# Performance work log

Hardware: AMD Instinct MI355X
Metric: run time of the kernel (lower is better)

Reference implementation:

```python
import jax, jax.numpy as jnp
import numpy as np
import math

D_MODEL = 1024
N_HEADS = 16
D_HEAD = D_MODEL // N_HEADS


def setup_inputs() -> dict:
    key = jax.random.key(0)
    ks = jax.random.split(key, 9)
    B, S = 4, 2048
    scale = 1.0 / math.sqrt(D_MODEL)
    x = jax.random.normal(ks[0], (B, S, D_MODEL), dtype=jnp.float32)
    # nn.Linear weights stored as [out, in]; we keep [in, out] for x @ W
    w_q = jax.random.uniform(ks[1], (D_MODEL, D_MODEL), jnp.float32, -scale, scale)
    b_q = jax.random.uniform(ks[2], (D_MODEL,), jnp.float32, -scale, scale)
    w_k = jax.random.uniform(ks[3], (D_MODEL, D_MODEL), jnp.float32, -scale, scale)
    b_k = jax.random.uniform(ks[4], (D_MODEL,), jnp.float32, -scale, scale)
    w_v = jax.random.uniform(ks[5], (D_MODEL, D_MODEL), jnp.float32, -scale, scale)
    b_v = jax.random.uniform(ks[6], (D_MODEL,), jnp.float32, -scale, scale)
    w_o = jax.random.uniform(ks[7], (D_MODEL, D_MODEL), jnp.float32, -scale, scale)
    b_o = jax.random.uniform(ks[8], (D_MODEL,), jnp.float32, -scale, scale)
    return {"x": x, "w_q": w_q, "b_q": b_q, "w_k": w_k, "b_k": b_k,
            "w_v": w_v, "b_v": b_v, "w_o": w_o, "b_o": b_o}


def reference(x, w_q, b_q, w_k, b_k, w_v, b_v, w_o, b_o):
    B, S, _ = x.shape
    def split_heads(t):  # [B,S,D] -> [B,H,S,Dh]
        return t.reshape(B, S, N_HEADS, D_HEAD).transpose(0, 2, 1, 3)
    q = split_heads(x @ w_q + b_q)
    k = split_heads(x @ w_k + b_k)
    v = split_heads(x @ w_v + b_v)
    scores = jnp.einsum('bhqd,bhkd->bhqk', q, k) / math.sqrt(D_HEAD)
    attn = jax.nn.softmax(scores, axis=-1)  # dropout p=0 -> identity
    ctx = jnp.einsum('bhqk,bhkd->bhqd', attn, v)
    ctx = ctx.transpose(0, 2, 1, 3).reshape(B, S, D_MODEL)
    return ctx @ w_o + b_o
```

## Files before the change

kernel.cpp:

```cpp
#include <hip/hip_runtime.h>
#include <hip/hip_bf16.h>

#define DM   1024
#define SEQ  2048
#define NH   16
#define DH   64
#define BH   64
#define MTOT 8192

typedef __attribute__((ext_vector_type(8))) short  short8;
typedef __attribute__((ext_vector_type(4))) short  short4v;
typedef __attribute__((ext_vector_type(4))) float  f32x4;
typedef __attribute__((ext_vector_type(4))) float  fvec4;
typedef unsigned short ushort_t;

#define AS1 __attribute__((address_space(1)))
#define AS3 __attribute__((address_space(3)))

static __device__ __forceinline__ unsigned short f2bf(float f){
  __bf16 h = (__bf16)f;
  return __builtin_bit_cast(unsigned short, h);
}

static __device__ __forceinline__ float fexp2(float x){
  float r;
  asm("v_exp_f32 %0, %1\n\ts_nop 0" : "=v"(r) : "v"(x));
  return r;
}

static __device__ __forceinline__ void gld16(const void* g, void* l){
  __builtin_amdgcn_global_load_lds((const AS1 int*)g, (AS3 int*)l, 16, 0, 0);
}

__global__ void k_cast_x(const float* __restrict__ x, ushort_t* __restrict__ xb){
  const size_t i = (size_t)blockIdx.x*256 + threadIdx.x;
  const fvec4* xv = (const fvec4*)x;
  fvec4 a = xv[2*i], b = xv[2*i+1];
  short8 r;
  #pragma unroll
  for (int j=0;j<4;++j) r[j]   = (short)f2bf(a[j]);
  #pragma unroll
  for (int j=0;j<4;++j) r[4+j] = (short)f2bf(b[j]);
  ((short8*)xb)[i] = r;
}

__global__ void k_cast_wt(const float* __restrict__ wq, const float* __restrict__ wk,
                          const float* __restrict__ wv, const float* __restrict__ wo,
                          ushort_t* __restrict__ wt){
  const int z = blockIdx.y;
  const float* W = (z==0)?wq:(z==1)?wk:(z==2)?wv:wo;
  ushort_t* Wt = wt + (size_t)z*DM*DM;
  const int k0 = (blockIdx.x & 15)*64, n0 = (blockIdx.x >> 4)*64;
  __shared__ float tile[64][65];
  const int t = threadIdx.x;
  #pragma unroll
  for (int it=0; it<4; ++it){
    int c = it*256 + t;
    int rr = c>>4, cc = c&15;
    fvec4 v = *(const fvec4*)(W + (size_t)(k0+rr)*DM + n0 + cc*4);
    #pragma unroll
    for (int j=0;j<4;++j) tile[cc*4+j][rr] = v[j];
  }
  __syncthreads();
  #pragma unroll
  for (int it=0; it<4; ++it){
    int c = it*256 + t;
    int nn = c>>4, kk = c&15;
    short4v r;
    #pragma unroll
    for (int j=0;j<4;++j) r[j] = (short)f2bf(tile[nn][kk*4+j]);
    *(short4v*)(Wt + (size_t)(n0+nn)*DM + k0 + kk*4) = r;
  }
}

template<int MODE>
__global__ __launch_bounds__(256, 2)
void k_gemm128(const ushort_t* __restrict__ A, const ushort_t* __restrict__ WtBase,
               const float* __restrict__ b0, const float* __restrict__ b1,
               const float* __restrict__ b2,
               ushort_t* __restrict__ obf, float* __restrict__ of32){
  const int z = blockIdx.z;
  const ushort_t* Wt = WtBase + (size_t)z*DM*DM;
  const float* bias = (z==0)? b0 : (z==1? b1 : b2);
  __shared__ ushort_t Al[128*32];
  __shared__ ushort_t Bl[128*32];
  const int t = threadIdx.x;
  const int wid = t>>6, l = t&63, g = l>>4, li = l&15;
  const int m0 = blockIdx.x*128, n0 = blockIdx.y*128;
  const int wr = (wid>>1)*64, wc = (wid&1)*64;
  const int srow = t>>2, schunk = (t&3)*8;

  f32x4 acc[4][4] = {};

  for (int kt = 0; kt < DM; kt += 32){
    __syncthreads();
    #pragma unroll
    for (int c = 0; c < 2; ++c){
      gld16(A  + (size_t)(m0 + c*64 + srow)*DM + kt + schunk, (char*)Al + c*4096 + wid*1024);
      gld16(Wt + (size_t)(n0 + c*64 + srow)*DM + kt + schunk, (char*)Bl + c*4096 + wid*1024);
    }
    __syncthreads();
    short8 af[4], bw[4];
    #pragma unroll
    for (int mt=0; mt<4; ++mt)
      af[mt] = *(const short8*)(Al + (wr + mt*16 + li)*32 + g*8);
    #pragma unroll
    for (int nt=0; nt<4; ++nt)
      bw[nt] = *(const short8*)(Bl + (wc + nt*16 + li)*32 + g*8);
    #pragma unroll
    for (int mt=0; mt<4; ++mt)
      #pragma unroll
      for (int nt=0; nt<4; ++nt)
        acc[mt][nt] = __builtin_amdgcn_mfma_f32_16x16x32_bf16(af[mt], bw[nt], acc[mt][nt], 0,0,0);
  }

  #pragma unroll
  for (int nt=0; nt<4; ++nt){
    const int n = n0 + wc + nt*16 + li;
    const float bn = bias[n];
    #pragma unroll
    for (int mt=0; mt<4; ++mt){
      #pragma unroll
      for (int r=0; r<4; ++r){
        const int m = m0 + wr + mt*16 + g*4 + r;
        const float v = acc[mt][nt][r] + bn;
        if constexpr (MODE==0){
          const int bb = m >> 11, s = m & 2047, h = n >> 6, d = n & 63;
          obf[(size_t)z*MTOT*DM + (((size_t)(bb*NH + h)*SEQ + s)*DH + d)] = f2bf(v);
        } else {
          of32[(size_t)m*DM + n] = v;
        }
      }
    }
  }
}

__global__ void k_transpose_v(const ushort_t* __restrict__ V, ushort_t* __restrict__ Vt){
  const int bh = blockIdx.y, s0 = blockIdx.x*64;
  __shared__ ushort_t tile[64][72];
  const int t = threadIdx.x;
  const ushort_t* Vh = V + (size_t)bh*SEQ*DH;
  ushort_t* Vth = Vt + (size_t)bh*DH*SEQ;
  #pragma unroll
  for (int it=0; it<2; ++it){
    int c = it*256 + t;
    int s_ = c>>3, d8 = (c&7)*8;
    short8 v = *(const short8*)(Vh + (size_t)(s0+s_)*DH + d8);
    #pragma unroll
    for (int j=0;j<8;++j) tile[d8+j][s_] = (ushort_t)v[j];
  }
  __syncthreads();
  #pragma unroll
  for (int it=0; it<2; ++it){
    int c = it*256 + t;
    int d_ = c>>3, s8 = (c&7)*8;
    short8 r = *(const short8*)(&tile[d_][s8]);
    *(short8*)(Vth + (size_t)d_*SEQ + s0 + s8) = r;
  }
}

#define CEXP 0.18033688011112042f

__global__ __launch_bounds__(256, 2)
void k_attn(const ushort_t* __restrict__ Qb, const ushort_t* __restrict__ Kb,
            const ushort_t* __restrict__ Vtb, ushort_t* __restrict__ ctx){
  const int bh = blockIdx.y, b = bh>>4, h = bh&15;
  const int t = threadIdx.x, wid = t>>6, l = t&63, g = l>>4, li = l&15;
  const int q0 = blockIdx.x*128;
  __shared__ ushort_t Kl[64*64];
  __shared__ ushort_t Vl[64*64];
  __shared__ ushort_t Pl[4][32*64];
  const ushort_t* Qh = Qb  + (size_t)bh*SEQ*DH;
  const ushort_t* Kh = Kb  + (size_t)bh*SEQ*DH;
  const ushort_t* Vh = Vtb + (size_t)bh*DH*SEQ;
  char* Plb = (char*)&Pl[wid][0];
  char* Klb = (char*)Kl;
  char* Vlb = (char*)Vl;

  short8 qf[2][2];
  #pragma unroll
  for (int nt=0; nt<2; ++nt)
    #pragma unroll
    for (int ks=0; ks<2; ++ks)
      qf[nt][ks] = *(const short8*)(Qh + (size_t)(q0 + wid*32 + nt*16 + li)*DH + ks*32 + g*8);

  f32x4 o[2][4] = {};
  float m_[2] = {-1e30f, -1e30f};
  float lsum[2] = {0.f, 0.f};

  for (int kv0 = 0; kv0 < SEQ; kv0 += 64){
    __syncthreads();
    #pragma unroll
    for (int it=0; it<2; ++it){
      int c = it*256 + t;
      int row = c>>3, ch = c&7;
      short8 kv_ = *(const short8*)(Kh + (size_t)(kv0+row)*DH + ch*8);
      *(short8*)(Klb + row*128 + ((ch ^ (row&7))<<4)) = kv_;
      short8 vv  = *(const short8*)(Vh + (size_t)row*SEQ + kv0 + ch*8);
      *(short8*)(Vlb + row*128 + ((ch ^ (row&7))<<4)) = vv;
    }
    __syncthreads();

    f32x4 s_[2][4] = {};
    #pragma unroll
    for (int ks=0; ks<2; ++ks){
      short8 af[4];
      #pragma unroll
      for (int mt=0; mt<4; ++mt){
        int row = mt*16 + li;
        af[mt] = *(const short8*)(Klb + row*128 + (((ks*4+g) ^ (row&7))<<4));
      }
      #pragma unroll
      for (int nt=0; nt<2; ++nt)
        #pragma unroll
        for (int mt=0; mt<4; ++mt)
          s_[nt][mt] = __builtin_amdgcn_mfma_f32_16x16x32_bf16(af[mt], qf[nt][ks], s_[nt][mt], 0,0,0);
    }

    float fac[2];
    #pragma unroll
    for (int nt=0; nt<2; ++nt){
      float tm = -1e30f;
      #pragma unroll
      for (int mt=0; mt<4; ++mt)
        #pragma unroll
        for (int r=0; r<4; ++r) tm = fmaxf(tm, s_[nt][mt][r]);
      tm = fmaxf(tm, __shfl_xor(tm, 16));
      tm = fmaxf(tm, __shfl_xor(tm, 32));
      const float mn = fmaxf(m_[nt], tm);
      fac[nt] = fexp2((m_[nt] - mn)*CEXP);
      m_[nt] = mn;
      float rs = 0.f;
      const int q = nt*16 + li;
      #pragma unroll
      for (int mt=0; mt<4; ++mt){
        short4v pk;
        #pragma unroll
        for (int r=0; r<4; ++r){
          float p = fexp2((s_[nt][mt][r] - mn)*CEXP);
          rs += p;
          pk[r] = (short)f2bf(p);
        }
        *(short4v*)(Plb + ((q*128 + (mt*16 + g*4)*2) ^ ((q&7)<<4))) = pk;
      }
      rs += __shfl_xor(rs, 16);
      rs += __shfl_xor(rs, 32);
      lsum[nt] = lsum[nt]*fac[nt] + rs;
    }

    #pragma unroll
    for (int qt=0; qt<2; ++qt)
      #pragma unroll
      for (int r=0; r<4; ++r){
        float fr = __shfl(fac[qt], g*4 + r);
        #pragma unroll
        for (int dt=0; dt<4; ++dt) o[qt][dt][r] *= fr;
      }

    #pragma unroll
    for (int ks=0; ks<2; ++ks){
      short8 pa[2];
      #pragma unroll
      for (int qt=0; qt<2; ++qt){
        int q = qt*16 + li;
        pa[qt] = *(const short8*)(Plb + ((q*128 + ks*64 + g*16) ^ ((q&7)<<4)));
      }
      short8 vb[4];
      #pragma unroll
      for (int dt=0; dt<4; ++dt){
        int d = dt*16 + li;
        vb[dt] = *(const short8*)(Vlb + d*128 + (((ks*4+g) ^ (d&7))<<4));
      }
      #pragma unroll
      for (int qt=0; qt<2; ++qt)
        #pragma unroll
        for (int dt=0; dt<4; ++dt)
          o[qt][dt] = __builtin_amdgcn_mfma_f32_16x16x32_bf16(pa[qt], vb[dt], o[qt][dt], 0,0,0);
    }
  }

  #pragma unroll
  for (int qt=0; qt<2; ++qt){
    const float inv = 1.f / lsum[qt];
    #pragma unroll
    for (int r=0; r<4; ++r){
      const float w = __shfl(inv, g*4 + r);
      const int qrow = q0 + wid*32 + qt*16 + g*4 + r;
      #pragma unroll
      for (int dt=0; dt<4; ++dt)
        ctx[((size_t)(b*SEQ + qrow))*DM + h*DH + dt*16 + li] = f2bf(o[qt][dt][r] * w);
    }
  }
}

extern "C" void kernel_launch(void* const* d_in, const int* in_sizes, int n_in,
                              void* d_out, int out_size, void* d_ws, size_t ws_size,
                              hipStream_t stream){
  const float* x  = (const float*)d_in[0];
  const float* wq = (const float*)d_in[1];
  const float* bq = (const float*)d_in[2];
  const float* wk = (const float*)d_in[3];
  const float* bk = (const float*)d_in[4];
  const float* wv = (const float*)d_in[5];
  const float* bv = (const float*)d_in[6];
  const float* wo = (const float*)d_in[7];
  const float* bo = (const float*)d_in[8];
  float* out = (float*)d_out;

  ushort_t* xb  = (ushort_t*)d_ws;
  ushort_t* wt  = xb  + (size_t)MTOT*DM;
  ushort_t* qkv = wt  + (size_t)4*DM*DM;
  ushort_t* vt  = qkv + (size_t)3*MTOT*DM;
  ushort_t* ctx = vt  + (size_t)MTOT*DM;

  k_cast_x<<<4096, 256, 0, stream>>>(x, xb);
  k_cast_wt<<<dim3(256,4), 256, 0, stream>>>(wq, wk, wv, wo, wt);
  k_gemm128<0><<<dim3(64,8,3), 256, 0, stream>>>(xb, wt, bq, bk, bv, qkv, nullptr);
  k_transpose_v<<<dim3(32,64), 256, 0, stream>>>(qkv + (size_t)2*MTOT*DM, vt);
  k_attn<<<dim3(16,64), 256, 0, stream>>>(qkv, qkv + (size_t)MTOT*DM, vt, ctx);
  k_gemm128<1><<<dim3(64,8,1), 256, 0, stream>>>(ctx, wt + (size_t)3*DM*DM, bo, bo, bo, nullptr, out);
}
```

Measured before the change: 322.2 us.

## Rewrite attention with 32x32 MFMA, register P, double-buffered async K/V loads

```diff
diff --git a/kernel.cpp b/kernel.cpp
--- a/kernel.cpp
+++ b/kernel.cpp
@@ -8,14 +8,19 @@
 #define BH   64
 #define MTOT 8192
 
-typedef __attribute__((ext_vector_type(8))) short  short8;
-typedef __attribute__((ext_vector_type(4))) short  short4v;
-typedef __attribute__((ext_vector_type(4))) float  f32x4;
-typedef __attribute__((ext_vector_type(4))) float  fvec4;
+typedef __attribute__((ext_vector_type(8)))  short short8;
+typedef __attribute__((ext_vector_type(4)))  short short4v;
+typedef __attribute__((ext_vector_type(4)))  float f32x4;
+typedef __attribute__((ext_vector_type(16))) float f32x16;
+typedef __attribute__((ext_vector_type(4)))  float fvec4;
+typedef __attribute__((ext_vector_type(4)))  int   i32x4;
 typedef unsigned short ushort_t;
 
 #define AS1 __attribute__((address_space(1)))
 #define AS3 __attribute__((address_space(3)))
+
+#define QSCALE 0.18033688011112042f
+#define THR_L2 11.541560327111707f
 
 static __device__ __forceinline__ unsigned short f2bf(float f){
   __bf16 h = (__bf16)f;
@@ -114,183 +119,197 @@
         acc[mt][nt] = __builtin_amdgcn_mfma_f32_16x16x32_bf16(af[mt], bw[nt], acc[mt][nt], 0,0,0);
   }
 
-  #pragma unroll
-  for (int nt=0; nt<4; ++nt){
-    const int n = n0 + wc + nt*16 + li;
-    const float bn = bias[n];
-    #pragma unroll
-    for (int mt=0; mt<4; ++mt){
-      #pragma unroll
-      for (int r=0; r<4; ++r){
-        const int m = m0 + wr + mt*16 + g*4 + r;
-        const float v = acc[mt][nt][r] + bn;
-        if constexpr (MODE==0){
-          const int bb = m >> 11, s = m & 2047, h = n >> 6, d = n & 63;
-          obf[(size_t)z*MTOT*DM + (((size_t)(bb*NH + h)*SEQ + s)*DH + d)] = f2bf(v);
-        } else {
-          of32[(size_t)m*DM + n] = v;
+  if constexpr (MODE==0){
+    if (z == 2){
+      ushort_t* vt = obf + (size_t)2*MTOT*DM;
+      #pragma unroll
+      for (int nt=0; nt<4; ++nt){
+        const int n = n0 + wc + nt*16 + li;
+        const float bn = bias[n];
+        const int h = n>>6, d = n&63;
+        #pragma unroll
+        for (int mt=0; mt<4; ++mt){
+          const int m = m0 + wr + mt*16 + g*4;
+          const int bb = m >> 11, s = m & 2047;
+          short4v pk;
+          #pragma unroll
+          for (int r=0; r<4; ++r) pk[r] = (short)f2bf(acc[mt][nt][r] + bn);
+          *(short4v*)(vt + (((size_t)(bb*NH + h)*DH + d)*SEQ + s)) = pk;
         }
       }
-    }
-  }
-}
-
-__global__ void k_transpose_v(const ushort_t* __restrict__ V, ushort_t* __restrict__ Vt){
-  const int bh = blockIdx.y, s0 = blockIdx.x*64;
-  __shared__ ushort_t tile[64][72];
-  const int t = threadIdx.x;
-  const ushort_t* Vh = V + (size_t)bh*SEQ*DH;
-  ushort_t* Vth = Vt + (size_t)bh*DH*SEQ;
-  #pragma unroll
-  for (int it=0; it<2; ++it){
-    int c = it*256 + t;
-    int s_ = c>>3, d8 = (c&7)*8;
-    short8 v = *(const short8*)(Vh + (size_t)(s0+s_)*DH + d8);
-    #pragma unroll
-    for (int j=0;j<8;++j) tile[d8+j][s_] = (ushort_t)v[j];
-  }
-  __syncthreads();
-  #pragma unroll
-  for (int it=0; it<2; ++it){
-    int c = it*256 + t;
-    int d_ = c>>3, s8 = (c&7)*8;
-    short8 r = *(const short8*)(&tile[d_][s8]);
-    *(short8*)(Vth + (size_t)d_*SEQ + s0 + s8) = r;
-  }
-}
-
-#define CEXP 0.18033688011112042f
+    } else {
+      const float sc = (z==0) ? QSCALE : 1.f;
+      #pragma unroll
+      for (int nt=0; nt<4; ++nt){
+        const int n = n0 + wc + nt*16 + li;
+        const float bn = bias[n];
+        #pragma unroll
+        for (int mt=0; mt<4; ++mt){
+          #pragma unroll
+          for (int r=0; r<4; ++r){
+            const int m = m0 + wr + mt*16 + g*4 + r;
+            const float v = (acc[mt][nt][r] + bn)*sc;
+            const int bb = m >> 11, s = m & 2047, h = n >> 6, d = n & 63;
+            obf[(size_t)z*MTOT*DM + (((size_t)(bb*NH + h)*SEQ + s)*DH + d)] = f2bf(v);
+          }
+        }
+      }
+    }
+  } else {
+    #pragma unroll
+    for (int nt=0; nt<4; ++nt){
+      const int n = n0 + wc + nt*16 + li;
+      const float bn = bias[n];
+      #pragma unroll
+      for (int mt=0; mt<4; ++mt){
+        #pragma unroll
+        for (int r=0; r<4; ++r){
+          const int m = m0 + wr + mt*16 + g*4 + r;
+          of32[(size_t)m*DM + n] = acc[mt][nt][r] + bn;
+        }
+      }
+    }
+  }
+}
 
 __global__ __launch_bounds__(256, 2)
 void k_attn(const ushort_t* __restrict__ Qb, const ushort_t* __restrict__ Kb,
             const ushort_t* __restrict__ Vtb, ushort_t* __restrict__ ctx){
   const int bh = blockIdx.y, b = bh>>4, h = bh&15;
-  const int t = threadIdx.x, wid = t>>6, l = t&63, g = l>>4, li = l&15;
-  const int q0 = blockIdx.x*128;
-  __shared__ ushort_t Kl[64*64];
-  __shared__ ushort_t Vl[64*64];
-  __shared__ ushort_t Pl[4][32*64];
+  const int t = threadIdx.x, wid = t>>6, lane = t&63;
+  const int lq = lane&31, hi = lane>>5;
+  const int qw = blockIdx.x*128 + wid*32;
+  __shared__ ushort_t Kl[2][64*64];
+  __shared__ ushort_t Vl[2][64*64];
   const ushort_t* Qh = Qb  + (size_t)bh*SEQ*DH;
   const ushort_t* Kh = Kb  + (size_t)bh*SEQ*DH;
   const ushort_t* Vh = Vtb + (size_t)bh*DH*SEQ;
-  char* Plb = (char*)&Pl[wid][0];
-  char* Klb = (char*)Kl;
-  char* Vlb = (char*)Vl;
-
-  short8 qf[2][2];
-  #pragma unroll
-  for (int nt=0; nt<2; ++nt)
-    #pragma unroll
-    for (int ks=0; ks<2; ++ks)
-      qf[nt][ks] = *(const short8*)(Qh + (size_t)(q0 + wid*32 + nt*16 + li)*DH + ks*32 + g*8);
-
-  f32x4 o[2][4] = {};
-  float m_[2] = {-1e30f, -1e30f};
-  float lsum[2] = {0.f, 0.f};
-
-  for (int kv0 = 0; kv0 < SEQ; kv0 += 64){
+
+  short8 qf[4];
+  #pragma unroll
+  for (int ks=0; ks<4; ++ks)
+    qf[ks] = *(const short8*)(Qh + (size_t)(qw+lq)*DH + ks*16 + hi*8);
+
+  f32x16 o0 = {}, o1 = {};
+  float m_ = 0.f, ls = 0.f;
+
+  const int srl = lane>>3, scp = lane&7;
+  #define STAGE(kv0, bi) do {                                              \
+    _Pragma("unroll")                                                      \
+    for (int i8=0; i8<2; ++i8){                                            \
+      const int row = wid*16 + i8*8 + srl;                                 \
+      const int c = scp ^ (row&7);                                         \
+      gld16(Kh + (size_t)((kv0)+row)*DH + c*8,                             \
+            (char*)&Kl[bi][0] + (wid*16+i8*8)*128);                        \
+      gld16(Vh + (size_t)row*SEQ + (kv0) + c*8,                            \
+            (char*)&Vl[bi][0] + (wid*16+i8*8)*128);                        \
+    }                                                                      \
+  } while(0)
+
+  STAGE(0, 0);
+  __syncthreads();
+
+  int cur = 0;
+  for (int t64 = 0; t64 < SEQ/64; ++t64){
+    if (t64 < SEQ/64 - 1){
+      if (cur) STAGE((t64+1)*64, 0); else STAGE((t64+1)*64, 1);
+    }
+    const char* Kb_ = (const char*)&Kl[cur][0];
+    const char* Vb_ = (const char*)&Vl[cur][0];
+
+    short8 kf[8];
+    #pragma unroll
+    for (int blk=0; blk<2; ++blk){
+      const int row = blk*32 + lq;
+      #pragma unroll
+      for (int ks=0; ks<4; ++ks)
+        kf[blk*4+ks] = *(const short8*)(Kb_ + row*128 + (((2*ks+hi) ^ (row&7))<<4));
+    }
+    f32x16 s0 = {}, s1 = {};
+    __builtin_amdgcn_s_setprio(1);
+    #pragma unroll
+    for (int ks=0; ks<4; ++ks){
+      s0 = __builtin_amdgcn_mfma_f32_32x32x16_bf16(kf[ks],   qf[ks], s0, 0,0,0);
+      s1 = __builtin_amdgcn_mfma_f32_32x32x16_bf16(kf[4+ks], qf[ks], s1, 0,0,0);
+    }
+    __builtin_amdgcn_s_setprio(0);
+
+    float tm = s0[0];
+    #pragma unroll
+    for (int r=1; r<16; ++r) tm = fmaxf(tm, s0[r]);
+    #pragma unroll
+    for (int r=0; r<16; ++r) tm = fmaxf(tm, s1[r]);
+    tm = fmaxf(tm, __shfl_xor(tm, 32));
+
+    if (!__all(tm <= m_ + THR_L2)){
+      const float mn = fmaxf(m_, tm);
+      const float fac = fexp2(m_ - mn);
+      m_ = mn; ls *= fac;
+      #pragma unroll
+      for (int r=0; r<16; ++r){
+        const float fr = __shfl(fac, (r&3) + 8*(r>>2) + 4*hi);
+        o0[r] *= fr; o1[r] *= fr;
+      }
+    }
+    #pragma unroll
+    for (int r=0; r<16; ++r){ float e = fexp2(s0[r]-m_); s0[r]=e; ls+=e; }
+    #pragma unroll
+    for (int r=0; r<16; ++r){ float e = fexp2(s1[r]-m_); s1[r]=e; ls+=e; }
+
+    short8 pa[4];
+    #pragma unroll
+    for (int blk=0; blk<2; ++blk){
+      #pragma unroll
+      for (int half=0; half<2; ++half){
+        i32x4 w;
+        #pragma unroll
+        for (int wp=0; wp<2; ++wp){
+          const int base = half*8 + 2*wp;
+          float a0 = blk ? s1[base]   : s0[base];
+          float a1 = blk ? s1[base+1] : s0[base+1];
+          float c0 = blk ? s1[base+4] : s0[base+4];
+          float c1 = blk ? s1[base+5] : s0[base+5];
+          int x, y;
+          asm("v_cvt_pk_bf16_f32 %0, %1, %2" : "=v"(x) : "v"(a0), "v"(a1));
+          asm("v_cvt_pk_bf16_f32 %0, %1, %2" : "=v"(y) : "v"(c0), "v"(c1));
+          asm("v_permlane32_swap_b32 %0, %1" : "+v"(x), "+v"(y));
+          w[wp] = x; w[2+wp] = y;
+        }
+        pa[blk*2+half] = __builtin_bit_cast(short8, w);
+      }
+    }
+
+    short8 vb[8];
+    #pragma unroll
+    for (int dblk=0; dblk<2; ++dblk){
+      const int row = dblk*32 + lq;
+      #pragma unroll
+      for (int ks=0; ks<4; ++ks)
+        vb[dblk*4+ks] = *(const short8*)(Vb_ + row*128 + (((2*ks+hi) ^ (row&7))<<4));
+    }
+    __builtin_amdgcn_s_setprio(1);
+    #pragma unroll
+    for (int ks=0; ks<4; ++ks){
+      o0 = __builtin_amdgcn_mfma_f32_32x32x16_bf16(pa[ks], vb[ks],   o0, 0,0,0);
+      o1 = __builtin_amdgcn_mfma_f32_32x32x16_bf16(pa[ks], vb[4+ks], o1, 0,0,0);
+    }
+    __builtin_amdgcn_s_setprio(0);
+
     __syncthreads();
-    #pragma unroll
-    for (int it=0; it<2; ++it){
-      int c = it*256 + t;
-      int row = c>>3, ch = c&7;
-      short8 kv_ = *(const short8*)(Kh + (size_t)(kv0+row)*DH + ch*8);
-      *(short8*)(Klb + row*128 + ((ch ^ (row&7))<<4)) = kv_;
-      short8 vv  = *(const short8*)(Vh + (size_t)row*SEQ + kv0 + ch*8);
-      *(short8*)(Vlb + row*128 + ((ch ^ (row&7))<<4)) = vv;
-    }
-    __syncthreads();
-
-    f32x4 s_[2][4] = {};
-    #pragma unroll
-    for (int ks=0; ks<2; ++ks){
-      short8 af[4];
-      #pragma unroll
-      for (int mt=0; mt<4; ++mt){
-        int row = mt*16 + li;
-        af[mt] = *(const short8*)(Klb + row*128 + (((ks*4+g) ^ (row&7))<<4));
-      }
-      #pragma unroll
-      for (int nt=0; nt<2; ++nt)
-        #pragma unroll
-        for (int mt=0; mt<4; ++mt)
-          s_[nt][mt] = __builtin_amdgcn_mfma_f32_16x16x32_bf16(af[mt], qf[nt][ks], s_[nt][mt], 0,0,0);
-    }
-
-    float fac[2];
-    #pragma unroll
-    for (int nt=0; nt<2; ++nt){
-      float tm = -1e30f;
-      #pragma unroll
-      for (int mt=0; mt<4; ++mt)
-        #pragma unroll
-        for (int r=0; r<4; ++r) tm = fmaxf(tm, s_[nt][mt][r]);
-      tm = fmaxf(tm, __shfl_xor(tm, 16));
-      tm = fmaxf(tm, __shfl_xor(tm, 32));
-      const float mn = fmaxf(m_[nt], tm);
-      fac[nt] = fexp2((m_[nt] - mn)*CEXP);
-      m_[nt] = mn;
-      float rs = 0.f;
-      const int q = nt*16 + li;
-      #pragma unroll
-      for (int mt=0; mt<4; ++mt){
-        short4v pk;
-        #pragma unroll
-        for (int r=0; r<4; ++r){
-          float p = fexp2((s_[nt][mt][r] - mn)*CEXP);
-          rs += p;
-          pk[r] = (short)f2bf(p);
-        }
-        *(short4v*)(Plb + ((q*128 + (mt*16 + g*4)*2) ^ ((q&7)<<4))) = pk;
-      }
-      rs += __shfl_xor(rs, 16);
-      rs += __shfl_xor(rs, 32);
-      lsum[nt] = lsum[nt]*fac[nt] + rs;
-    }
-
-    #pragma unroll
-    for (int qt=0; qt<2; ++qt)
-      #pragma unroll
-      for (int r=0; r<4; ++r){
-        float fr = __shfl(fac[qt], g*4 + r);
-        #pragma unroll
-        for (int dt=0; dt<4; ++dt) o[qt][dt][r] *= fr;
-      }
-
-    #pragma unroll
-    for (int ks=0; ks<2; ++ks){
-      short8 pa[2];
-      #pragma unroll
-      for (int qt=0; qt<2; ++qt){
-        int q = qt*16 + li;
-        pa[qt] = *(const short8*)(Plb + ((q*128 + ks*64 + g*16) ^ ((q&7)<<4)));
-      }
-      short8 vb[4];
-      #pragma unroll
-      for (int dt=0; dt<4; ++dt){
-        int d = dt*16 + li;
-        vb[dt] = *(const short8*)(Vlb + d*128 + (((ks*4+g) ^ (d&7))<<4));
-      }
-      #pragma unroll
-      for (int qt=0; qt<2; ++qt)
-        #pragma unroll
-        for (int dt=0; dt<4; ++dt)
-          o[qt][dt] = __builtin_amdgcn_mfma_f32_16x16x32_bf16(pa[qt], vb[dt], o[qt][dt], 0,0,0);
-    }
-  }
-
-  #pragma unroll
-  for (int qt=0; qt<2; ++qt){
-    const float inv = 1.f / lsum[qt];
-    #pragma unroll
-    for (int r=0; r<4; ++r){
-      const float w = __shfl(inv, g*4 + r);
-      const int qrow = q0 + wid*32 + qt*16 + g*4 + r;
-      #pragma unroll
-      for (int dt=0; dt<4; ++dt)
-        ctx[((size_t)(b*SEQ + qrow))*DM + h*DH + dt*16 + li] = f2bf(o[qt][dt][r] * w);
-    }
-  }
+    cur ^= 1;
+  }
+
+  ls += __shfl_xor(ls, 32);
+  const float inv = 1.f / ls;
+  #pragma unroll
+  for (int r=0; r<16; ++r){
+    const float ir = __shfl(inv, (r&3) + 8*(r>>2) + 4*hi);
+    const int qrow = qw + (r&3) + 8*(r>>2) + 4*hi;
+    ushort_t* dst = ctx + ((size_t)(b*SEQ + qrow))*DM + h*DH;
+    dst[lq]    = f2bf(o0[r]*ir);
+    dst[32+lq] = f2bf(o1[r]*ir);
+  }
+  #undef STAGE
 }
 
 extern "C" void kernel_launch(void* const* d_in, const int* in_sizes, int n_in,
@@ -310,13 +329,11 @@
   ushort_t* xb  = (ushort_t*)d_ws;
   ushort_t* wt  = xb  + (size_t)MTOT*DM;
   ushort_t* qkv = wt  + (size_t)4*DM*DM;
-  ushort_t* vt  = qkv + (size_t)3*MTOT*DM;
-  ushort_t* ctx = vt  + (size_t)MTOT*DM;
+  ushort_t* ctx = qkv + (size_t)3*MTOT*DM;
 
   k_cast_x<<<4096, 256, 0, stream>>>(x, xb);
   k_cast_wt<<<dim3(256,4), 256, 0, stream>>>(wq, wk, wv, wo, wt);
   k_gemm128<0><<<dim3(64,8,3), 256, 0, stream>>>(xb, wt, bq, bk, bv, qkv, nullptr);
-  k_transpose_v<<<dim3(32,64), 256, 0, stream>>>(qkv + (size_t)2*MTOT*DM, vt);
-  k_attn<<<dim3(16,64), 256, 0, stream>>>(qkv, qkv + (size_t)MTOT*DM, vt, ctx);
+  k_attn<<<dim3(16,64), 256, 0, stream>>>(qkv, qkv + (size_t)MTOT*DM, qkv + (size_t)2*MTOT*DM, ctx);
   k_gemm128<1><<<dim3(64,8,1), 256, 0, stream>>>(ctx, wt + (size_t)3*DM*DM, bo, bo, bo, nullptr, out);
 }
```

Result: faster. 284.0 us (-11.9%).
